# Kernel tuning notes

Hardware: AMD Instinct MI355X
Metric: run time of the kernel (lower is better)

Reference implementation:

```python
import jax, jax.numpy as jnp
import numpy as np

N = 16384       # number of nodes
E = 65536       # total children (avg 4 per node)
D = 512         # input_size
H = 512         # hidden_size


def setup_inputs() -> dict:
    key = jax.random.key(0)
    ks = jax.random.split(key, 12)
    x = jax.random.normal(ks[0], (N, D), dtype=jnp.float32)
    prev_c = jax.random.normal(ks[1], (E, H), dtype=jnp.float32)
    prev_h = jax.random.normal(ks[2], (E, H), dtype=jnp.float32)
    seg_ids = jnp.sort(jax.random.randint(ks[3], (E,), 0, N, dtype=jnp.int32))
    s = 0.02
    Wc = jax.random.normal(ks[4], (3 * H, D + H), dtype=jnp.float32) * s
    bc = jnp.zeros((3 * H,), dtype=jnp.float32)
    Wwf = jax.random.normal(ks[5], (H, D), dtype=jnp.float32) * s
    bwf = jnp.ones((H,), dtype=jnp.float32)
    Wuf = jax.random.normal(ks[6], (H, H), dtype=jnp.float32) * s
    buf = jnp.ones((H,), dtype=jnp.float32)
    return {"x": x, "prev_c": prev_c, "prev_h": prev_h, "seg_ids": seg_ids,
            "Wc": Wc, "bc": bc, "Wwf": Wwf, "bwf": bwf, "Wuf": Wuf, "buf": buf}


def reference(x, prev_c, prev_h, seg_ids, Wc, bc, Wwf, bwf, Wuf, buf):
    # h_tilde[j] = sum of children hidden states of node j
    h_tilde = jax.ops.segment_sum(prev_h, seg_ids, num_segments=N,
                                  indices_are_sorted=True)  # [N, H]
    big = jnp.concatenate([x, h_tilde], axis=1) @ Wc.T + bc   # [N, 3H]
    z_i, z_o, z_u = jnp.split(big, 3, axis=1)
    # dropout is identity in eval mode
    f_inputs = x @ Wwf.T + bwf            # [N, H]
    f_hiddens = prev_h @ Wuf.T + buf      # [E, H]
    f_jk = jax.nn.sigmoid(f_inputs[seg_ids] + f_hiddens)  # [E, H]
    fc_term = jax.ops.segment_sum(f_jk * prev_c, seg_ids, num_segments=N,
                                  indices_are_sorted=True)  # [N, H]
    c = jax.nn.sigmoid(z_i) * jnp.tanh(z_u) + fc_term
    h = jax.nn.sigmoid(z_o) * jnp.tanh(c)
    return (c, h)
```

## Files before the change

kernel.cpp:

```cpp
#include <hip/hip_runtime.h>
#include <hip/hip_bf16.h>

#define NN 16384
#define EE 65536
#define DD 512
#define HH 512

typedef short bf16x8 __attribute__((ext_vector_type(8)));
typedef float f32x4 __attribute__((ext_vector_type(4)));
typedef float float4v __attribute__((ext_vector_type(4)));
typedef unsigned short u16x4 __attribute__((ext_vector_type(4)));

__device__ __forceinline__ float b2f(unsigned short u) {
  union { unsigned int i; float f; } v; v.i = ((unsigned int)u) << 16; return v.f;
}
__device__ __forceinline__ unsigned short f2b(float f) {
  union { float f; unsigned int i; } v; v.f = f;
  unsigned int lsb = (v.i >> 16) & 1u;
  v.i += 0x7fffu + lsb;
  return (unsigned short)(v.i >> 16);
}
__device__ __forceinline__ float sigm(float x) { return 1.f / (1.f + expf(-x)); }

__device__ __forceinline__ void async16(const void* g, void* l) {
  __builtin_amdgcn_global_load_lds(
      (const __attribute__((address_space(1))) void*)g,
      (__attribute__((address_space(3))) void*)l, 16, 0, 0);
}

__global__ void k_segstart(const int* __restrict__ seg, int* __restrict__ out) {
  int j = blockIdx.x * blockDim.x + threadIdx.x;
  if (j > NN) return;
  int lo = 0, hi = EE;
  while (lo < hi) { int mid = (lo + hi) >> 1; if (seg[mid] < j) lo = mid + 1; else hi = mid; }
  out[j] = lo;
}

__global__ void k_cast_x(const float* __restrict__ x, unsigned short* __restrict__ Abig) {
  int idx = (blockIdx.x * 256 + threadIdx.x) * 4;
  if (idx >= NN * DD) return;
  int row = idx >> 9, col = idx & 511;
  float4v v = *(const float4v*)&x[idx];
  u16x4 o; o.x = f2b(v.x); o.y = f2b(v.y); o.z = f2b(v.z); o.w = f2b(v.w);
  *(u16x4*)&Abig[(size_t)row * 1024 + col] = o;
}

__global__ __launch_bounds__(256) void k_htilde(const float* __restrict__ prev_h,
                                                const int* __restrict__ segstart,
                                                unsigned short* __restrict__ Abig) {
  int j = blockIdx.x;
  int t = threadIdx.x;
  int s = segstart[j], e = segstart[j + 1];
  float a0 = 0.f, a1 = 0.f;
  for (int i = s; i < e; ++i) {
    a0 += prev_h[(size_t)i * 512 + t];
    a1 += prev_h[(size_t)i * 512 + t + 256];
  }
  Abig[(size_t)j * 1024 + 512 + t] = f2b(a0);
  Abig[(size_t)j * 1024 + 512 + 256 + t] = f2b(a1);
}

__global__ void k_build_wbig(const float* __restrict__ Wc, const float* __restrict__ Wwf,
                             unsigned short* __restrict__ Wbig) {
  int idx = (blockIdx.x * 256 + threadIdx.x) * 4;
  if (idx >= 2048 * 1024) return;
  int row = idx >> 10, col = idx & 1023;
  u16x4 o;
  if (row < 1536) {
    float4v v = *(const float4v*)&Wc[(size_t)row * 1024 + col];
    o.x = f2b(v.x); o.y = f2b(v.y); o.z = f2b(v.z); o.w = f2b(v.w);
  } else if (col < 512) {
    float4v v = *(const float4v*)&Wwf[(size_t)(row - 1536) * 512 + col];
    o.x = f2b(v.x); o.y = f2b(v.y); o.z = f2b(v.z); o.w = f2b(v.w);
  } else {
    o.x = 0; o.y = 0; o.z = 0; o.w = 0;
  }
  *(u16x4*)&Wbig[idx] = o;
}

__global__ void k_cast(const float* __restrict__ s, unsigned short* __restrict__ d, int n) {
  int idx = (blockIdx.x * 256 + threadIdx.x) * 4;
  if (idx >= n) return;
  float4v v = *(const float4v*)&s[idx];
  u16x4 o; o.x = f2b(v.x); o.y = f2b(v.y); o.z = f2b(v.z); o.w = f2b(v.w);
  *(u16x4*)&d[idx] = o;
}

#define BM 128
#define BN 128
#define BK 32

__global__ __launch_bounds__(256) void gemm_bt_kernel(
    const unsigned short* __restrict__ A, const unsigned short* __restrict__ B,
    unsigned short* __restrict__ C, int M, int Nout, int K) {
  __shared__ unsigned short lA[BM * BK];
  __shared__ unsigned short lB[BN * BK];
  const int t = threadIdx.x;
  const int w = t >> 6;
  const int l = t & 63;
  const int wr = w >> 1;
  const int wc = w & 1;
  const int row0 = blockIdx.y * BM;
  const int col0 = blockIdx.x * BN;
  const int lr = l & 15;
  const int lk = (l >> 4) * 8;
  const int crow = t >> 2;
  const int ccol = (t & 3) * 8;

  f32x4 acc[4][4] = {};

  for (int k0 = 0; k0 < K; k0 += BK) {
    async16(A + (size_t)(row0 + crow) * K + (k0 + ccol), &lA[(size_t)(w * 64) * 8]);
    async16(A + (size_t)(row0 + 64 + crow) * K + (k0 + ccol), &lA[(size_t)(256 + w * 64) * 8]);
    async16(B + (size_t)(col0 + crow) * K + (k0 + ccol), &lB[(size_t)(w * 64) * 8]);
    async16(B + (size_t)(col0 + 64 + crow) * K + (k0 + ccol), &lB[(size_t)(256 + w * 64) * 8]);
    __syncthreads();

    bf16x8 af[4], bfv[4];
#pragma unroll
    for (int m = 0; m < 4; ++m)
      af[m] = *(const bf16x8*)&lA[(wr * 64 + m * 16 + lr) * BK + lk];
#pragma unroll
    for (int n = 0; n < 4; ++n)
      bfv[n] = *(const bf16x8*)&lB[(wc * 64 + n * 16 + lr) * BK + lk];
#pragma unroll
    for (int m = 0; m < 4; ++m)
#pragma unroll
      for (int n = 0; n < 4; ++n)
        acc[m][n] = __builtin_amdgcn_mfma_f32_16x16x32_bf16(af[m], bfv[n], acc[m][n], 0, 0, 0);
    __syncthreads();
  }

#pragma unroll
  for (int m = 0; m < 4; ++m) {
    const int rb = row0 + wr * 64 + m * 16 + (l >> 4) * 4;
#pragma unroll
    for (int n = 0; n < 4; ++n) {
      const int cb = col0 + wc * 64 + n * 16 + lr;
#pragma unroll
      for (int r = 0; r < 4; ++r)
        C[(size_t)(rb + r) * Nout + cb] = f2b(acc[m][n][r]);
    }
  }
}

__global__ __launch_bounds__(256) void k_final(
    const unsigned short* __restrict__ big, const unsigned short* __restrict__ fh,
    const float* __restrict__ prev_c, const int* __restrict__ segstart,
    const float* __restrict__ bc, const float* __restrict__ bwf,
    const float* __restrict__ bufv, float* __restrict__ out) {
  int j = blockIdx.x;
  int t = threadIdx.x;
  int h = t * 2;
  int s = segstart[j], e = segstart[j + 1];
  const unsigned short* bj = big + (size_t)j * 2048;
  float zi0 = b2f(bj[h])        + bc[h];
  float zi1 = b2f(bj[h + 1])    + bc[h + 1];
  float zo0 = b2f(bj[512 + h])  + bc[512 + h];
  float zo1 = b2f(bj[513 + h])  + bc[513 + h];
  float zu0 = b2f(bj[1024 + h]) + bc[1024 + h];
  float zu1 = b2f(bj[1025 + h]) + bc[1025 + h];
  float fi0 = b2f(bj[1536 + h]) + bwf[h]     + bufv[h];
  float fi1 = b2f(bj[1537 + h]) + bwf[h + 1] + bufv[h + 1];
  float fc0 = 0.f, fc1 = 0.f;
  for (int i = s; i < e; ++i) {
    unsigned int ff = *(const unsigned int*)&fh[(size_t)i * 512 + h];
    float2 pc = *(const float2*)&prev_c[(size_t)i * 512 + h];
    fc0 += sigm(fi0 + b2f((unsigned short)(ff & 0xffffu))) * pc.x;
    fc1 += sigm(fi1 + b2f((unsigned short)(ff >> 16)))     * pc.y;
  }
  float c0 = sigm(zi0) * tanhf(zu0) + fc0;
  float c1 = sigm(zi1) * tanhf(zu1) + fc1;
  size_t ob = (size_t)j * 512 + h;
  out[ob]     = c0;
  out[ob + 1] = c1;
  out[(size_t)NN * 512 + ob]     = sigm(zo0) * tanhf(c0);
  out[(size_t)NN * 512 + ob + 1] = sigm(zo1) * tanhf(c1);
}

extern "C" void kernel_launch(void* const* d_in, const int* in_sizes, int n_in,
                              void* d_out, int out_size, void* d_ws, size_t ws_size,
                              hipStream_t stream) {
  const float* x      = (const float*)d_in[0];
  const float* prev_c = (const float*)d_in[1];
  const float* prev_h = (const float*)d_in[2];
  const int*   seg    = (const int*)d_in[3];
  const float* Wc     = (const float*)d_in[4];
  const float* bc     = (const float*)d_in[5];
  const float* Wwf    = (const float*)d_in[6];
  const float* bwf    = (const float*)d_in[7];
  const float* Wuf    = (const float*)d_in[8];
  const float* bufv   = (const float*)d_in[9];

  char* ws = (char*)d_ws;
  size_t off = 0;
  unsigned short* Abig   = (unsigned short*)(ws + off); off += (size_t)NN * 1024 * 2;
  unsigned short* Wbig   = (unsigned short*)(ws + off); off += (size_t)2048 * 1024 * 2;
  unsigned short* bigout = (unsigned short*)(ws + off); off += (size_t)NN * 2048 * 2;
  unsigned short* phb    = (unsigned short*)(ws + off); off += (size_t)EE * 512 * 2;
  unsigned short* Wufb   = (unsigned short*)(ws + off); off += (size_t)512 * 512 * 2;
  unsigned short* fhout  = (unsigned short*)(ws + off); off += (size_t)EE * 512 * 2;
  int* segstart          = (int*)(ws + off);            off += (size_t)(NN + 1) * 4;

  k_segstart<<<(NN + 256) / 256, 256, 0, stream>>>(seg, segstart);
  k_cast_x<<<(NN * DD / 4 + 255) / 256, 256, 0, stream>>>(x, Abig);
  k_htilde<<<NN, 256, 0, stream>>>(prev_h, segstart, Abig);
  k_build_wbig<<<(2048 * 1024 / 4 + 255) / 256, 256, 0, stream>>>(Wc, Wwf, Wbig);
  k_cast<<<(EE * HH / 4 + 255) / 256, 256, 0, stream>>>(prev_h, phb, EE * HH);
  k_cast<<<(HH * HH / 4 + 255) / 256, 256, 0, stream>>>(Wuf, Wufb, HH * HH);

  gemm_bt_kernel<<<dim3(2048 / BN, NN / BM), 256, 0, stream>>>(Abig, Wbig, bigout, NN, 2048, 1024);
  gemm_bt_kernel<<<dim3(512 / BN, EE / BM), 256, 0, stream>>>(phb, Wufb, fhout, EE, 512, 512);

  k_final<<<NN, 256, 0, stream>>>(bigout, fhout, prev_c, segstart, bc, bwf, bufv, (float*)d_out);
}
```

Measured before the change: 563.9 us.

## Fuse prev_h bf16 cast into segment sum; widen GEMM K-tile, swizzle blocks

```diff
diff --git a/kernel.cpp b/kernel.cpp
--- a/kernel.cpp
+++ b/kernel.cpp
@@ -45,16 +45,20 @@
   *(u16x4*)&Abig[(size_t)row * 1024 + col] = o;
 }
 
-__global__ __launch_bounds__(256) void k_htilde(const float* __restrict__ prev_h,
-                                                const int* __restrict__ segstart,
-                                                unsigned short* __restrict__ Abig) {
+__global__ __launch_bounds__(256) void k_castsum(const float* __restrict__ prev_h,
+                                                 const int* __restrict__ segstart,
+                                                 unsigned short* __restrict__ phb,
+                                                 unsigned short* __restrict__ Abig) {
   int j = blockIdx.x;
   int t = threadIdx.x;
   int s = segstart[j], e = segstart[j + 1];
   float a0 = 0.f, a1 = 0.f;
   for (int i = s; i < e; ++i) {
-    a0 += prev_h[(size_t)i * 512 + t];
-    a1 += prev_h[(size_t)i * 512 + t + 256];
+    float v0 = prev_h[(size_t)i * 512 + t];
+    float v1 = prev_h[(size_t)i * 512 + 256 + t];
+    phb[(size_t)i * 512 + t] = f2b(v0);
+    phb[(size_t)i * 512 + 256 + t] = f2b(v1);
+    a0 += v0; a1 += v1;
   }
   Abig[(size_t)j * 1024 + 512 + t] = f2b(a0);
   Abig[(size_t)j * 1024 + 512 + 256 + t] = f2b(a1);
@@ -88,7 +92,7 @@
 
 #define BM 128
 #define BN 128
-#define BK 32
+#define BK 64
 
 __global__ __launch_bounds__(256) void gemm_bt_kernel(
     const unsigned short* __restrict__ A, const unsigned short* __restrict__ B,
@@ -100,34 +104,46 @@
   const int l = t & 63;
   const int wr = w >> 1;
   const int wc = w & 1;
-  const int row0 = blockIdx.y * BM;
-  const int col0 = blockIdx.x * BN;
+
+  const int nwg = gridDim.x * gridDim.y;
+  int bid = blockIdx.y * gridDim.x + blockIdx.x;
+  bid = (bid & 7) * (nwg >> 3) + (bid >> 3);
+  const int row0 = (bid / gridDim.x) * BM;
+  const int col0 = (bid % gridDim.x) * BN;
+
   const int lr = l & 15;
   const int lk = (l >> 4) * 8;
-  const int crow = t >> 2;
-  const int ccol = (t & 3) * 8;
+  const int crow = t >> 3;
+  const int ccol = (t & 7) * 8;
+  const int wbase = w * 512;
 
   f32x4 acc[4][4] = {};
 
   for (int k0 = 0; k0 < K; k0 += BK) {
-    async16(A + (size_t)(row0 + crow) * K + (k0 + ccol), &lA[(size_t)(w * 64) * 8]);
-    async16(A + (size_t)(row0 + 64 + crow) * K + (k0 + ccol), &lA[(size_t)(256 + w * 64) * 8]);
-    async16(B + (size_t)(col0 + crow) * K + (k0 + ccol), &lB[(size_t)(w * 64) * 8]);
-    async16(B + (size_t)(col0 + 64 + crow) * K + (k0 + ccol), &lB[(size_t)(256 + w * 64) * 8]);
+#pragma unroll
+    for (int c = 0; c < 4; ++c) {
+      async16(A + (size_t)(row0 + c * 32 + crow) * K + (k0 + ccol), &lA[c * 2048 + wbase]);
+      async16(B + (size_t)(col0 + c * 32 + crow) * K + (k0 + ccol), &lB[c * 2048 + wbase]);
+    }
     __syncthreads();
 
-    bf16x8 af[4], bfv[4];
-#pragma unroll
-    for (int m = 0; m < 4; ++m)
-      af[m] = *(const bf16x8*)&lA[(wr * 64 + m * 16 + lr) * BK + lk];
-#pragma unroll
-    for (int n = 0; n < 4; ++n)
-      bfv[n] = *(const bf16x8*)&lB[(wc * 64 + n * 16 + lr) * BK + lk];
-#pragma unroll
-    for (int m = 0; m < 4; ++m)
+    bf16x8 af[2][4], bfv[2][4];
+#pragma unroll
+    for (int ks = 0; ks < 2; ++ks) {
+#pragma unroll
+      for (int m = 0; m < 4; ++m)
+        af[ks][m] = *(const bf16x8*)&lA[(wr * 64 + m * 16 + lr) * BK + ks * 32 + lk];
 #pragma unroll
       for (int n = 0; n < 4; ++n)
-        acc[m][n] = __builtin_amdgcn_mfma_f32_16x16x32_bf16(af[m], bfv[n], acc[m][n], 0, 0, 0);
+        bfv[ks][n] = *(const bf16x8*)&lB[(wc * 64 + n * 16 + lr) * BK + ks * 32 + lk];
+    }
+#pragma unroll
+    for (int ks = 0; ks < 2; ++ks)
+#pragma unroll
+      for (int m = 0; m < 4; ++m)
+#pragma unroll
+        for (int n = 0; n < 4; ++n)
+          acc[m][n] = __builtin_amdgcn_mfma_f32_16x16x32_bf16(af[ks][m], bfv[ks][n], acc[m][n], 0, 0, 0);
     __syncthreads();
   }
 
@@ -204,9 +220,8 @@
 
   k_segstart<<<(NN + 256) / 256, 256, 0, stream>>>(seg, segstart);
   k_cast_x<<<(NN * DD / 4 + 255) / 256, 256, 0, stream>>>(x, Abig);
-  k_htilde<<<NN, 256, 0, stream>>>(prev_h, segstart, Abig);
+  k_castsum<<<NN, 256, 0, stream>>>(prev_h, segstart, phb, Abig);
   k_build_wbig<<<(2048 * 1024 / 4 + 255) / 256, 256, 0, stream>>>(Wc, Wwf, Wbig);
-  k_cast<<<(EE * HH / 4 + 255) / 256, 256, 0, stream>>>(prev_h, phb, EE * HH);
   k_cast<<<(HH * HH / 4 + 255) / 256, 256, 0, stream>>>(Wuf, Wufb, HH * HH);
 
   gemm_bt_kernel<<<dim3(2048 / BN, NN / BM), 256, 0, stream>>>(Abig, Wbig, bigout, NN, 2048, 1024);
```

Result: no change. 566.2 us (+0.4%).
